# Optimization experiments

Measured on AMD Instinct MI355X. Metric: run time of the kernel, lower is better.

The kernel has to match this reference:

```python
import jax, jax.numpy as jnp
import numpy as np


def _rotate_nearest(img, theta):
    """Rotate a batch of images (B, C, H, W) counterclockwise by theta radians
    about the image center, nearest-neighbor sampling, zero fill outside
    (matches torchvision rotate defaults: InterpolationMode.NEAREST, expand=False)."""
    B, C, H, W = img.shape
    cy = (H - 1) / 2.0
    cx = (W - 1) / 2.0
    ys = jnp.arange(H, dtype=jnp.float32) - cy
    xs = jnp.arange(W, dtype=jnp.float32) - cx
    yg, xg = jnp.meshgrid(ys, xs, indexing="ij")  # (H, W)
    c = jnp.cos(theta)
    s = jnp.sin(theta)
    # inverse affine map: output pixel -> source pixel
    x_src = c * xg + s * yg + cx
    y_src = -s * xg + c * yg + cy
    xi = jnp.round(x_src).astype(jnp.int32)
    yi = jnp.round(y_src).astype(jnp.int32)
    valid = (xi >= 0) & (xi < W) & (yi >= 0) & (yi < H)
    xi = jnp.clip(xi, 0, W - 1)
    yi = jnp.clip(yi, 0, H - 1)
    out = img[:, :, yi, xi]  # gather -> (B, C, H, W)
    return jnp.where(valid, out, jnp.zeros((), img.dtype))


def reference(image, kernel_size):
    # image: (B, C, H, W, A); A = num_angles
    B, C, H, W, A = image.shape
    angle_increment = 360.0 / A
    offsets = (jnp.arange(A) % kernel_size).astype(jnp.float32)
    # torch code calls rotate(slice, -angle_increment * relative_offset) in degrees
    thetas = jnp.deg2rad(-angle_increment * offsets)  # (A,)
    img_a = jnp.moveaxis(image, -1, 0)  # (A, B, C, H, W)
    rot = jax.vmap(_rotate_nearest, in_axes=(0, 0))(img_a, thetas)  # (A, B, C, H, W)
    rot = jnp.moveaxis(rot, 0, -1)  # (B, C, H, W, A)
    # MaxPool3d(kernel=(1,1,k)) == non-overlapping max over windows of k along angle dim
    pooled = rot.reshape(B, C, H, W, A // kernel_size, kernel_size).max(axis=-1)
    return pooled  # (B, C, H, W, A // kernel_size)


def setup_inputs() -> dict:
    key = jax.random.key(0)
    image = jax.random.normal(key, (8, 16, 128, 128, 24), dtype=jnp.float32)
    return {"image": image, "kernel_size": 4}
```

## Files before the change

### kernel.cpp

```cpp
#include <hip/hip_runtime.h>
#include <math.h>


#pragma clang fp contract(off)

#define BB 8
#define CC 16
#define HH 128
#define WW 128
#define AA 24
#define KK 4
#define GG 6

__global__ __launch_bounds__(256) void glp_rotation_pool_kernel(
    const float* __restrict__ img, float* __restrict__ out) {
  int blk = blockIdx.x;
  int xcd = blk & 7;
  int i   = blk >> 3;
  int bc  = xcd * 16 + (i >> 6);
  int rp  = i & 63;

  int tid = threadIdx.x;
  int y = rp * 2 + (tid >> 7);
  int x = tid & 127;

  const float cx = 63.5f;
  const float cy = 63.5f;

  float xg = (float)x - cx;
  float yg = (float)y - cy;

  const float* base = img + (size_t)bc * (HH * WW * AA);

  float res[GG];
#pragma unroll
  for (int g = 0; g < GG; ++g) res[g] = -INFINITY;

#pragma unroll
  for (int k = 0; k < KK; ++k) {
    float tdeg  = -15.0f * (float)k;
    float theta = tdeg * 0.017453292519943295f;
    float cth = (float)cos((double)theta);
    float sth = (float)sin((double)theta);

    float xs = cth * xg + sth * yg + cx;
    float ys = (-sth) * xg + cth * yg + cy;

    int xi = (int)rintf(xs);
    int yi = (int)rintf(ys);

    bool valid = ((unsigned)xi < (unsigned)WW) & ((unsigned)yi < (unsigned)HH);
    int xc = min(max(xi, 0), WW - 1);
    int yc = min(max(yi, 0), HH - 1);

    const float* p = base + ((size_t)(yc * WW + xc)) * AA + k;
#pragma unroll
    for (int g = 0; g < GG; ++g) {
      float v = p[g * KK];
      v = valid ? v : 0.0f;
      res[g] = fmaxf(res[g], v);
    }
  }

  float* o = out + ((size_t)bc * (HH * WW) + (size_t)(y * WW + x)) * GG;
#pragma unroll
  for (int g = 0; g < GG; ++g) o[g] = res[g];
}

extern "C" void kernel_launch(void* const* d_in, const int* in_sizes, int n_in,
                              void* d_out, int out_size, void* d_ws, size_t ws_size,
                              hipStream_t stream) {
  const float* img = (const float*)d_in[0];
  float* out = (float*)d_out;
  dim3 grid(BB * CC * HH * WW / 256);
  dim3 block(256);
  glp_rotation_pool_kernel<<<grid, block, 0, stream>>>(img, out);
}
```

Measured before the change: 323.0 us.

## Map one thread per output element for coalesced stores and gathers

Reassigns work so each thread computes a single (pixel, group) output instead of all six groups for one pixel. A 192-thread block covers 32 pixels by 6 groups, so output stores become fully contiguous and the gather loads for neighboring groups fall in adjacent addresses. The aim is to remove the strided 6-float-per-thread stores and scattered loads. In exchange the rotation coordinates are recomputed six times per pixel, there are more blocks, and an integer divide by 6 is added.

```diff
diff --git a/kernel.cpp b/kernel.cpp
--- a/kernel.cpp
+++ b/kernel.cpp
@@ -12,17 +12,20 @@
 #define KK 4
 #define GG 6
 
-__global__ __launch_bounds__(256) void glp_rotation_pool_kernel(
+__global__ __launch_bounds__(192) void glp_rotation_pool_kernel(
     const float* __restrict__ img, float* __restrict__ out) {
   int blk = blockIdx.x;
   int xcd = blk & 7;
   int i   = blk >> 3;
-  int bc  = xcd * 16 + (i >> 6);
-  int rp  = i & 63;
+  int bc  = (xcd << 4) | (i >> 9);
+  int s   = i & 511;
+  int y   = s >> 2;
+  int x0  = (s & 3) << 5;
 
   int tid = threadIdx.x;
-  int y = rp * 2 + (tid >> 7);
-  int x = tid & 127;
+  int pix = (unsigned)tid / 6u;
+  int g   = (unsigned)tid - 6u * pix;
+  int x   = x0 + pix;
 
   const float cx = 63.5f;
   const float cy = 63.5f;
@@ -32,9 +35,7 @@
 
   const float* base = img + (size_t)bc * (HH * WW * AA);
 
-  float res[GG];
-#pragma unroll
-  for (int g = 0; g < GG; ++g) res[g] = -INFINITY;
+  float res = -INFINITY;
 
 #pragma unroll
   for (int k = 0; k < KK; ++k) {
@@ -53,18 +54,13 @@
     int xc = min(max(xi, 0), WW - 1);
     int yc = min(max(yi, 0), HH - 1);
 
-    const float* p = base + ((size_t)(yc * WW + xc)) * AA + k;
-#pragma unroll
-    for (int g = 0; g < GG; ++g) {
-      float v = p[g * KK];
-      v = valid ? v : 0.0f;
-      res[g] = fmaxf(res[g], v);
-    }
+    float v = base[((size_t)(yc * WW + xc)) * AA + (k + 4 * g)];
+    v = valid ? v : 0.0f;
+    res = fmaxf(res, v);
   }
 
-  float* o = out + ((size_t)bc * (HH * WW) + (size_t)(y * WW + x)) * GG;
-#pragma unroll
-  for (int g = 0; g < GG; ++g) o[g] = res[g];
+  size_t obase = ((size_t)bc * (HH * WW) + (size_t)y * WW + x0) * GG;
+  out[obase + tid] = res;
 }
 
 extern "C" void kernel_launch(void* const* d_in, const int* in_sizes, int n_in,
@@ -72,7 +68,7 @@
                               hipStream_t stream) {
   const float* img = (const float*)d_in[0];
   float* out = (float*)d_out;
-  dim3 grid(BB * CC * HH * WW / 256);
-  dim3 block(256);
+  dim3 grid(BB * CC * HH * 4);
+  dim3 block(192);
   glp_rotation_pool_kernel<<<grid, block, 0, stream>>>(img, out);
 }
```

Measured after the change: 309.8 us. 4.1% less time.

## Pre-pack input into bf16 per-rotation vectors before rotate-gather-pool

Applied to the files above, without the earlier changes.

Adds a reformat pass that converts each pixel's 24 angle channels to bf16 and packs the six channels used by each rotation offset into one 16-byte vector. The gather kernel then does one vector load per rotation instead of six strided scalar loads, and writes its output as float2. This trades an extra full read/write pass over the input for fewer and narrower gather loads, and bf16 rounding changes the output values.

```diff
diff --git a/kernel.cpp b/kernel.cpp
--- a/kernel.cpp
+++ b/kernel.cpp
@@ -4,20 +4,50 @@
 
 #pragma clang fp contract(off)
 
-#define BB 8
-#define CC 16
 #define HH 128
 #define WW 128
 #define AA 24
 #define KK 4
 #define GG 6
+#define NSLICE 128
+#define PX_PER_SLICE (HH * WW)
+#define NPX (NSLICE * PX_PER_SLICE)
 
-__global__ __launch_bounds__(256) void glp_rotation_pool_kernel(
-    const float* __restrict__ img, float* __restrict__ out) {
+typedef unsigned int uint;
+
+static __device__ __forceinline__ unsigned short f2bf(float f) {
+  uint u = __float_as_uint(f);
+  u += 0x7FFFu + ((u >> 16) & 1u);
+  return (unsigned short)(u >> 16);
+}
+
+__global__ __launch_bounds__(256) void reformat_kernel(
+    const float* __restrict__ img, uint4* __restrict__ T) {
+  int px = blockIdx.x * 256 + threadIdx.x;
+  const float4* rec = (const float4*)img + (size_t)px * 6;
+  float4 c0 = rec[0], c1 = rec[1], c2 = rec[2], c3 = rec[3], c4 = rec[4],
+         c5 = rec[5];
+  float ch[24] = {c0.x, c0.y, c0.z, c0.w, c1.x, c1.y, c1.z, c1.w,
+                  c2.x, c2.y, c2.z, c2.w, c3.x, c3.y, c3.z, c3.w,
+                  c4.x, c4.y, c4.z, c4.w, c5.x, c5.y, c5.z, c5.w};
+  uint4* dst = T + (size_t)px * 4;
+#pragma unroll
+  for (int k = 0; k < KK; ++k) {
+    uint4 w;
+    w.x = (uint)f2bf(ch[k])      | ((uint)f2bf(ch[k + 4])  << 16);
+    w.y = (uint)f2bf(ch[k + 8])  | ((uint)f2bf(ch[k + 12]) << 16);
+    w.z = (uint)f2bf(ch[k + 16]) | ((uint)f2bf(ch[k + 20]) << 16);
+    w.w = 0;
+    dst[k] = w;
+  }
+}
+
+__global__ __launch_bounds__(256) void rotate_pool_kernel(
+    const uint4* __restrict__ T, float* __restrict__ out) {
   int blk = blockIdx.x;
   int xcd = blk & 7;
   int i   = blk >> 3;
-  int bc  = xcd * 16 + (i >> 6);
+  int bc  = (xcd << 4) | (i >> 6);
   int rp  = i & 63;
 
   int tid = threadIdx.x;
@@ -26,15 +56,13 @@
 
   const float cx = 63.5f;
   const float cy = 63.5f;
-
   float xg = (float)x - cx;
   float yg = (float)y - cy;
 
-  const float* base = img + (size_t)bc * (HH * WW * AA);
+  const uint4* base = T + (size_t)bc * PX_PER_SLICE * 4;
 
-  float res[GG];
-#pragma unroll
-  for (int g = 0; g < GG; ++g) res[g] = -INFINITY;
+  float r0 = -INFINITY, r1 = -INFINITY, r2 = -INFINITY,
+        r3 = -INFINITY, r4 = -INFINITY, r5 = -INFINITY;
 
 #pragma unroll
   for (int k = 0; k < KK; ++k) {
@@ -53,18 +81,26 @@
     int xc = min(max(xi, 0), WW - 1);
     int yc = min(max(yi, 0), HH - 1);
 
-    const float* p = base + ((size_t)(yc * WW + xc)) * AA + k;
-#pragma unroll
-    for (int g = 0; g < GG; ++g) {
-      float v = p[g * KK];
-      v = valid ? v : 0.0f;
-      res[g] = fmaxf(res[g], v);
-    }
+    uint4 t = base[(size_t)(yc * WW + xc) * 4 + k];
+    float g0 = __uint_as_float(t.x << 16);
+    float g1 = __uint_as_float(t.x & 0xFFFF0000u);
+    float g2 = __uint_as_float(t.y << 16);
+    float g3 = __uint_as_float(t.y & 0xFFFF0000u);
+    float g4 = __uint_as_float(t.z << 16);
+    float g5 = __uint_as_float(t.z & 0xFFFF0000u);
+    r0 = fmaxf(r0, valid ? g0 : 0.0f);
+    r1 = fmaxf(r1, valid ? g1 : 0.0f);
+    r2 = fmaxf(r2, valid ? g2 : 0.0f);
+    r3 = fmaxf(r3, valid ? g3 : 0.0f);
+    r4 = fmaxf(r4, valid ? g4 : 0.0f);
+    r5 = fmaxf(r5, valid ? g5 : 0.0f);
   }
 
-  float* o = out + ((size_t)bc * (HH * WW) + (size_t)(y * WW + x)) * GG;
-#pragma unroll
-  for (int g = 0; g < GG; ++g) o[g] = res[g];
+  size_t px = (size_t)bc * PX_PER_SLICE + (size_t)y * WW + x;
+  float2* o2 = (float2*)(out + px * GG);
+  o2[0] = make_float2(r0, r1);
+  o2[1] = make_float2(r2, r3);
+  o2[2] = make_float2(r4, r5);
 }
 
 extern "C" void kernel_launch(void* const* d_in, const int* in_sizes, int n_in,
@@ -72,7 +108,9 @@
                               hipStream_t stream) {
   const float* img = (const float*)d_in[0];
   float* out = (float*)d_out;
-  dim3 grid(BB * CC * HH * WW / 256);
+  uint4* T = (uint4*)d_ws;
+
   dim3 block(256);
-  glp_rotation_pool_kernel<<<grid, block, 0, stream>>>(img, out);
+  reformat_kernel<<<dim3(NPX / 256), block, 0, stream>>>(img, T);
+  rotate_pool_kernel<<<dim3(NPX / 256), block, 0, stream>>>(T, out);
 }
```

After: 356.3 us. 1.1x slower.
